# Kernel tuning notes

Measured on AMD Instinct MI355X. Metric: run time of the kernel, lower is better.

## Reference

```python
import jax, jax.numpy as jnp
import numpy as np

N_GRAPHS = 262144
NPG = 6          # players per Rocket League graph
N_NODES = N_GRAPHS * NPG
HIDDEN = 32
FEAT = 4


def _build_edges():
    # fully-connected directed edges within each 6-node graph (30 per graph)
    s, d = np.meshgrid(np.arange(NPG), np.arange(NPG), indexing='ij')
    m = s != d
    ts, td = s[m], d[m]                      # [30]
    off = (np.arange(N_GRAPHS, dtype=np.int64) * NPG)[:, None]
    src = (ts[None, :] + off).reshape(-1)
    dst = (td[None, :] + off).reshape(-1)
    return np.stack([src, dst]).astype(np.int32)  # [2, E]


def setup_inputs() -> dict:
    key = jax.random.key(0)
    ks = jax.random.split(key, 10)
    edge_index = jnp.asarray(_build_edges())
    E = edge_index.shape[1]
    batch = jnp.asarray(np.repeat(np.arange(N_GRAPHS, dtype=np.int32), NPG))
    return {
        'x': jax.random.normal(ks[0], (N_NODES, FEAT), dtype=jnp.float32),
        'edge_index': edge_index,
        'edge_weight': jax.random.uniform(ks[1], (E,), dtype=jnp.float32),
        'batch': batch,
        'W1': jax.random.normal(ks[2], (FEAT, HIDDEN), dtype=jnp.float32) * 0.5,
        'b1': jax.random.normal(ks[3], (HIDDEN,), dtype=jnp.float32) * 0.1,
        'W2': jax.random.normal(ks[4], (HIDDEN, HIDDEN), dtype=jnp.float32) * 0.18,
        'b2': jax.random.normal(ks[5], (HIDDEN,), dtype=jnp.float32) * 0.1,
        'Wo': jax.random.normal(ks[6], (HIDDEN, 1), dtype=jnp.float32) * 0.18,
        'bo': jax.random.normal(ks[7], (1,), dtype=jnp.float32) * 0.1,
        'Wb': jax.random.normal(ks[8], (HIDDEN, 1), dtype=jnp.float32) * 0.18,
        'bb': jax.random.normal(ks[9], (1,), dtype=jnp.float32) * 0.1,
    }


def _gcn_conv(x, W, b, src, dst, w, n_nodes):
    # PyG GCNConv: symmetric normalization with self-loops already appended
    h = x @ W                                            # [N, out]
    deg = jax.ops.segment_sum(w, dst, num_segments=n_nodes)
    dinv = jnp.where(deg > 0, jax.lax.rsqrt(deg), 0.0)
    norm = dinv[src] * w * dinv[dst]                     # [E]
    agg = jax.ops.segment_sum(norm[:, None] * h[src], dst, num_segments=n_nodes)
    return agg + b


def reference(x, edge_index, edge_weight, batch, W1, b1, W2, b2, Wo, bo, Wb, bb):
    n = x.shape[0]
    loop = jnp.arange(n, dtype=edge_index.dtype)
    src = jnp.concatenate([edge_index[0], loop])
    dst = jnp.concatenate([edge_index[1], loop])
    w = jnp.concatenate([edge_weight, jnp.ones((n,), edge_weight.dtype)])

    h = jax.nn.relu(_gcn_conv(x, W1, b1, src, dst, w, n))
    h = jax.nn.relu(_gcn_conv(h, W2, b2, src, dst, w, n))

    # global mean pool by graph
    n_graphs = N_GRAPHS
    sums = jax.ops.segment_sum(h, batch, num_segments=n_graphs)
    cnt = jax.ops.segment_sum(jnp.ones((n,), h.dtype), batch, num_segments=n_graphs)
    pooled = sums / jnp.maximum(cnt, 1.0)[:, None]       # [G, 32]

    orange = jax.nn.sigmoid(pooled @ Wo + bo)            # [G, 1]
    blue = jax.nn.sigmoid(pooled @ Wb + bb)              # [G, 1]
    return orange, blue
```

## Files before the change

kernel.cpp:

```cpp
#include <hip/hip_runtime.h>
#include <hip/hip_bf16.h>

#define G_TOTAL 262144
#define ITERS   2
#define WAVES   4
#define NBLK    4096

typedef short s8v __attribute__((ext_vector_type(8)));
typedef float f4v __attribute__((ext_vector_type(4)));

#define MFMA16(a,b,c) __builtin_amdgcn_mfma_f32_16x16x32_bf16(a,b,c,0,0,0)

__device__ __forceinline__ unsigned short f2bf(float f){
    union { __hip_bfloat16 h; unsigned short u; } cv;
    cv.h = __float2bfloat16(f);
    return cv.u;
}
__device__ __forceinline__ unsigned int pk2(float a, float b){
    return (unsigned int)f2bf(a) | ((unsigned int)f2bf(b) << 16);
}

union FragU { s8v s; uint4 u; };

#define ARENA 7952

__global__ __launch_bounds__(256, 4)
void gcn_wave(const float* __restrict__ x,
              const float* __restrict__ ew,
              const float* __restrict__ W1,
              const float* __restrict__ b1,
              const float* __restrict__ W2,
              const float* __restrict__ b2,
              const float* __restrict__ Wo,
              const float* __restrict__ bo,
              const float* __restrict__ Wb,
              const float* __restrict__ bb,
              float* __restrict__ out)
{
    __shared__ __align__(16) unsigned char LDS[WAVES*ARENA];
    __shared__ float obuf[2][64];

    const int tid = threadIdx.x;
    const int w   = tid >> 6;
    const int l   = tid & 63;
    const int lr  = l & 15;
    const int lq  = l >> 4;

    unsigned char* AR = LDS + w*ARENA;
    unsigned short* h1RW  = (unsigned short*)AR;
    float*          rsumW = (float*)AR;
    unsigned short* actTW = (unsigned short*)(AR + 3456);
    unsigned int*   bandB = (unsigned int*)(AR + 6784);

    #pragma unroll
    for (int i = 0; i < 5; ++i) { const int k = l + 64*i; if (k < 292) bandB[k] = 0u; }

    const int gB = l / 6, dB = l - 6*gB;
    const bool bOK = (l < 48);
    const int gBc = bOK ? gB : 0;
    const int dBc = bOK ? dB : 0;
    int eoff0, eoff1, eoff2, eoff3, eoff4, eoff5;
    {
        int eo[6];
        #pragma unroll
        for (int s = 0; s < 6; ++s)
            eo[s] = (s == dBc) ? gBc*30
                               : gBc*30 + s*5 + (dBc - (dBc > s ? 1 : 0));
        eoff0=eo[0]; eoff1=eo[1]; eoff2=eo[2]; eoff3=eo[3]; eoff4=eo[4]; eoff5=eo[5];
    }
    const int sbB   = 6*gBc;
    const int bcell = bOK ? l : 0;
    int bAddr[3];
    #pragma unroll
    for (int nt = 0; nt < 3; ++nt) {
        const int r  = 16*nt + lr;
        const int g  = r / 6;
        const int s0 = (8*nt + 8*lq - 6*g) >> 1;
        bAddr[nt] = (s0 < -3 || s0 > 2) ? 288 : (6*r + s0);
    }

    s8v w1f[2], w2f[2];
    #pragma unroll
    for (int cn = 0; cn < 2; ++cn) {
        #pragma unroll
        for (int e = 0; e < 8; ++e) {
            const int k = lq*8 + e, col = lr + 16*cn;
            w1f[cn][e] = (k < 4) ? (short)f2bf(W1[k*32 + col]) : (short)0;
            w2f[cn][e] = (short)f2bf(W2[k*32 + col]);
        }
    }
    f4v cb1[2], cb2[2];
    float wor[2][4], wbr[2][4];
    #pragma unroll
    for (int mtc = 0; mtc < 2; ++mtc)
        #pragma unroll
        for (int j = 0; j < 4; ++j) {
            const int ch = 16*mtc + lq*4 + j;
            cb1[mtc][j] = b1[ch];  cb2[mtc][j] = b2[ch];
            wor[mtc][j] = Wo[ch];  wbr[mtc][j] = Wb[ch];
        }
    const float boS = bo[0], bbS = bb[0];

    const long base = (long)blockIdx.x*(32*ITERS) + w*8;

    float evl[2][6];
    uint2 xB[2][3];

    {
        const long gb30 = base*30;
        evl[0][0] = ew[gb30 + eoff0];  evl[0][1] = ew[gb30 + eoff1];
        evl[0][2] = ew[gb30 + eoff2];  evl[0][3] = ew[gb30 + eoff3];
        evl[0][4] = ew[gb30 + eoff4];  evl[0][5] = ew[gb30 + eoff5];
        if (lq == 0) {
            const float* xp = x + base*24;
            #pragma unroll
            for (int mt = 0; mt < 3; ++mt) {
                const float4 xv = *(const float4*)(xp + (16*mt + lr)*4);
                xB[0][mt] = make_uint2(pk2(xv.x, xv.y), pk2(xv.z, xv.w));
            }
        }
    }

    #pragma unroll
    for (int it = 0; it < ITERS; ++it) {
        const int  cbuf = it & 1, nbuf = cbuf ^ 1;
        const long gbW  = base + it*32;

        if (it + 1 < ITERS) {
            const long gb30 = (gbW + 32)*30;
            evl[nbuf][0] = ew[gb30 + eoff0];  evl[nbuf][1] = ew[gb30 + eoff1];
            evl[nbuf][2] = ew[gb30 + eoff2];  evl[nbuf][3] = ew[gb30 + eoff3];
            evl[nbuf][4] = ew[gb30 + eoff4];  evl[nbuf][5] = ew[gb30 + eoff5];
            if (lq == 0) {
                const float* xp = x + (gbW + 32)*24;
                #pragma unroll
                for (int mt = 0; mt < 3; ++mt) {
                    const float4 xv = *(const float4*)(xp + (16*mt + lr)*4);
                    xB[nbuf][mt] = make_uint2(pk2(xv.x, xv.y), pk2(xv.z, xv.w));
                }
            }
        }

        #pragma unroll
        for (int mt = 0; mt < 3; ++mt) {
            s8v a = {0,0,0,0,0,0,0,0};
            if (lq == 0) {
                FragU ua; ua.u = make_uint4(xB[cbuf][mt].x, xB[cbuf][mt].y, 0u, 0u);
                a = ua.s;
            }
            #pragma unroll
            for (int cn = 0; cn < 2; ++cn) {
                f4v z = {0.f,0.f,0.f,0.f};
                f4v t = MFMA16(a, w1f[cn], z);
                *(uint2*)(actTW + (16*cn + lr)*52 + 16*mt + 4*lq) =
                    make_uint2(pk2(t[0],t[1]), pk2(t[2],t[3]));
            }
        }

        {
            const float ws0 = (dB==0) ? 1.0f : evl[cbuf][0];
            const float ws1 = (dB==1) ? 1.0f : evl[cbuf][1];
            const float ws2 = (dB==2) ? 1.0f : evl[cbuf][2];
            const float ws3 = (dB==3) ? 1.0f : evl[cbuf][3];
            const float ws4 = (dB==4) ? 1.0f : evl[cbuf][4];
            const float ws5 = (dB==5) ? 1.0f : evl[cbuf][5];
            const float dd  = rsqrtf(ws0+ws1+ws2+ws3+ws4+ws5);
            const float dv0 = __shfl(dd, sbB+0), dv1 = __shfl(dd, sbB+1);
            const float dv2 = __shfl(dd, sbB+2), dv3 = __shfl(dd, sbB+3);
            const float dv4 = __shfl(dd, sbB+4), dv5 = __shfl(dd, sbB+5);
            if (bOK) {
                *(uint2*)(bandB + bcell*6) =
                    make_uint2(pk2(dd*ws0*dv0, dd*ws1*dv1), pk2(dd*ws2*dv2, dd*ws3*dv3));
                bandB[bcell*6 + 2] = pk2(dd*ws4*dv4, dd*ws5*dv5);
            }
        }

        uint4 bfrv[3];
        #pragma unroll
        for (int nt = 0; nt < 3; ++nt) {
            {
                const unsigned int* bp = bandB + bAddr[nt];
                bfrv[nt] = make_uint4(bp[0], bp[1], bp[2], bp[3]);
            }
            FragU ub; ub.u = bfrv[nt];
            #pragma unroll
            for (int mtc = 0; mtc < 2; ++mtc) {
                FragU ua;
                const unsigned short* ap = actTW + (16*mtc + lr)*52 + 8*nt + 8*lq;
                const uint2 a0 = *(const uint2*)ap;
                const uint2 a1 = *(const uint2*)(ap + 4);
                ua.u = make_uint4(a0.x, a0.y, a1.x, a1.y);
                f4v dD = MFMA16(ua.s, ub.s, cb1[mtc]);
                const float h0 = fmaxf(dD[0], 0.f);
                const float h1v= fmaxf(dD[1], 0.f);
                const float h2v= fmaxf(dD[2], 0.f);
                const float h3v= fmaxf(dD[3], 0.f);
                *(uint2*)(h1RW + (16*nt + lr)*36 + 16*mtc + 4*lq) =
                    make_uint2(pk2(h0,h1v), pk2(h2v,h3v));
            }
        }

        #pragma unroll
        for (int mt = 0; mt < 3; ++mt) {
            FragU ua;
            const unsigned short* hp = h1RW + (16*mt + lr)*36 + 8*lq;
            const uint2 h0 = *(const uint2*)hp;
            const uint2 h1p= *(const uint2*)(hp + 4);
            ua.u = make_uint4(h0.x, h0.y, h1p.x, h1p.y);
            const s8v a = ua.s;
            #pragma unroll
            for (int cn = 0; cn < 2; ++cn) {
                f4v z = {0.f,0.f,0.f,0.f};
                f4v t = MFMA16(a, w2f[cn], z);
                *(uint2*)(actTW + (16*cn + lr)*52 + 16*mt + 4*lq) =
                    make_uint2(pk2(t[0],t[1]), pk2(t[2],t[3]));
            }
        }

        #pragma unroll
        for (int nt = 0; nt < 3; ++nt) {
            FragU ub; ub.u = bfrv[nt];
            float po = 0.f, pb = 0.f;
            #pragma unroll
            for (int mtc = 0; mtc < 2; ++mtc) {
                FragU ua;
                const unsigned short* ap = actTW + (16*mtc + lr)*52 + 8*nt + 8*lq;
                const uint2 a0 = *(const uint2*)ap;
                const uint2 a1 = *(const uint2*)(ap + 4);
                ua.u = make_uint4(a0.x, a0.y, a1.x, a1.y);
                f4v dD = MFMA16(ua.s, ub.s, cb2[mtc]);
                #pragma unroll
                for (int j = 0; j < 4; ++j) {
                    const float h = fmaxf(dD[j], 0.f);
                    po += h * wor[mtc][j];
                    pb += h * wbr[mtc][j];
                }
            }
            po += __shfl_xor(po, 16);  po += __shfl_xor(po, 32);
            pb += __shfl_xor(pb, 16);  pb += __shfl_xor(pb, 32);
            if (lq == 0)      rsumW[16*nt + lr]      = po;
            else if (lq == 1) rsumW[48 + 16*nt + lr] = pb;
        }

        if (l < 16) {
            const int head = l >> 3, gl = l & 7;
            const float* rs = rsumW + head*48 + gl*6;
            const float2 a0 = *(const float2*)rs;
            const float2 a1 = *(const float2*)(rs + 2);
            const float2 a2 = *(const float2*)(rs + 4);
            const float s6 = a0.x+a0.y+a1.x+a1.y+a2.x+a2.y;
            const float zz = s6*(1.f/6.f) + (head ? bbS : boS);
            obuf[head][it*32 + w*8 + gl] = 1.f/(1.f + __expf(-zz));
        }
    }

    __syncthreads();
    if (tid < 128) {
        const int head = tid >> 6, idx = tid & 63;
        out[(long)head*G_TOTAL + (long)blockIdx.x*64 + idx] = obuf[head][idx];
    }
}

extern "C" void kernel_launch(void* const* d_in, const int* in_sizes, int n_in,
                              void* d_out, int out_size, void* d_ws, size_t ws_size,
                              hipStream_t stream)
{
    const float* x  = (const float*)d_in[0];
    const float* ew = (const float*)d_in[2];
    const float* W1 = (const float*)d_in[4];
    const float* b1 = (const float*)d_in[5];
    const float* W2 = (const float*)d_in[6];
    const float* b2 = (const float*)d_in[7];
    const float* Wo = (const float*)d_in[8];
    const float* bo = (const float*)d_in[9];
    const float* Wb = (const float*)d_in[10];
    const float* bb = (const float*)d_in[11];
    float* out = (float*)d_out;

    hipLaunchKernelGGL(gcn_wave, dim3(NBLK), dim3(256), 0, stream,
                       x, ew, W1, b1, W2, b2, Wo, bo, Wb, bb, out);
}
```

Measured before the change: 44.53 us.

## Keep transformed activations in registers and remap band fragments to match

Result: slower. 47.52 us (+6.7%).

```diff
diff --git a/kernel.cpp b/kernel.cpp
--- a/kernel.cpp
+++ b/kernel.cpp
@@ -22,7 +22,7 @@
 
 union FragU { s8v s; uint4 u; };
 
-#define ARENA 7952
+#define ARENA 4624
 
 __global__ __launch_bounds__(256, 4)
 void gcn_wave(const float* __restrict__ x,
@@ -49,8 +49,7 @@
     unsigned char* AR = LDS + w*ARENA;
     unsigned short* h1RW  = (unsigned short*)AR;
     float*          rsumW = (float*)AR;
-    unsigned short* actTW = (unsigned short*)(AR + 3456);
-    unsigned int*   bandB = (unsigned int*)(AR + 6784);
+    unsigned int*   bandB = (unsigned int*)(AR + 3456);
 
     #pragma unroll
     for (int i = 0; i < 5; ++i) { const int k = l + 64*i; if (k < 292) bandB[k] = 0u; }
@@ -70,13 +69,18 @@
     }
     const int sbB   = 6*gBc;
     const int bcell = bOK ? l : 0;
-    int bAddr[3];
+    const bool lq3  = (lq == 3);
+    int bLo[3], bHi[3];
     #pragma unroll
     for (int nt = 0; nt < 3; ++nt) {
+        const int aSel = (nt == 0) ? 0 : ((nt == 2) ? 1 : (lq3 ? 0 : 1));
+        const int bSel = (nt == 0) ? 1 : ((nt == 2) ? 2 : (lq3 ? 1 : 2));
         const int r  = 16*nt + lr;
         const int g  = r / 6;
-        const int s0 = (8*nt + 8*lq - 6*g) >> 1;
-        bAddr[nt] = (s0 < -3 || s0 > 2) ? 288 : (6*r + s0);
+        const int sL = (16*aSel + 4*lq - 6*g) >> 1;
+        const int sH = (16*bSel + 4*lq - 6*g) >> 1;
+        bLo[nt] = (sL < -3 || sL > 4) ? 288 : 6*r + sL;
+        bHi[nt] = (sH < -3 || sH > 4) ? 288 : 6*r + sH;
     }
 
     s8v w1f[2], w2f[2];
@@ -141,6 +145,7 @@
             }
         }
 
+        uint2 t1pk[3][2];
         #pragma unroll
         for (int mt = 0; mt < 3; ++mt) {
             s8v a = {0,0,0,0,0,0,0,0};
@@ -152,8 +157,7 @@
             for (int cn = 0; cn < 2; ++cn) {
                 f4v z = {0.f,0.f,0.f,0.f};
                 f4v t = MFMA16(a, w1f[cn], z);
-                *(uint2*)(actTW + (16*cn + lr)*52 + 16*mt + 4*lq) =
-                    make_uint2(pk2(t[0],t[1]), pk2(t[2],t[3]));
+                t1pk[mt][cn] = make_uint2(pk2(t[0],t[1]), pk2(t[2],t[3]));
             }
         }
 
@@ -178,18 +182,18 @@
         uint4 bfrv[3];
         #pragma unroll
         for (int nt = 0; nt < 3; ++nt) {
-            {
-                const unsigned int* bp = bandB + bAddr[nt];
-                bfrv[nt] = make_uint4(bp[0], bp[1], bp[2], bp[3]);
-            }
+            bfrv[nt] = make_uint4(bandB[bLo[nt]], bandB[bLo[nt]+1],
+                                  bandB[bHi[nt]], bandB[bHi[nt]+1]);
             FragU ub; ub.u = bfrv[nt];
             #pragma unroll
             for (int mtc = 0; mtc < 2; ++mtc) {
-                FragU ua;
-                const unsigned short* ap = actTW + (16*mtc + lr)*52 + 8*nt + 8*lq;
-                const uint2 a0 = *(const uint2*)ap;
-                const uint2 a1 = *(const uint2*)(ap + 4);
-                ua.u = make_uint4(a0.x, a0.y, a1.x, a1.y);
+                const uint2 lo = (nt==0) ? t1pk[0][mtc]
+                               : (nt==2) ? t1pk[1][mtc]
+                               : (lq3 ? t1pk[0][mtc] : t1pk[1][mtc]);
+                const uint2 hi = (nt==0) ? t1pk[1][mtc]
+                               : (nt==2) ? t1pk[2][mtc]
+                               : (lq3 ? t1pk[1][mtc] : t1pk[2][mtc]);
+                FragU ua; ua.u = make_uint4(lo.x, lo.y, hi.x, hi.y);
                 f4v dD = MFMA16(ua.s, ub.s, cb1[mtc]);
                 const float h0 = fmaxf(dD[0], 0.f);
                 const float h1v= fmaxf(dD[1], 0.f);
@@ -200,6 +204,7 @@
             }
         }
 
+        uint2 t2pk[3][2];
         #pragma unroll
         for (int mt = 0; mt < 3; ++mt) {
             FragU ua;
@@ -212,8 +217,7 @@
             for (int cn = 0; cn < 2; ++cn) {
                 f4v z = {0.f,0.f,0.f,0.f};
                 f4v t = MFMA16(a, w2f[cn], z);
-                *(uint2*)(actTW + (16*cn + lr)*52 + 16*mt + 4*lq) =
-                    make_uint2(pk2(t[0],t[1]), pk2(t[2],t[3]));
+                t2pk[mt][cn] = make_uint2(pk2(t[0],t[1]), pk2(t[2],t[3]));
             }
         }
 
@@ -223,11 +227,13 @@
             float po = 0.f, pb = 0.f;
             #pragma unroll
             for (int mtc = 0; mtc < 2; ++mtc) {
-                FragU ua;
-                const unsigned short* ap = actTW + (16*mtc + lr)*52 + 8*nt + 8*lq;
-                const uint2 a0 = *(const uint2*)ap;
-                const uint2 a1 = *(const uint2*)(ap + 4);
-                ua.u = make_uint4(a0.x, a0.y, a1.x, a1.y);
+                const uint2 lo = (nt==0) ? t2pk[0][mtc]
+                               : (nt==2) ? t2pk[1][mtc]
+                               : (lq3 ? t2pk[0][mtc] : t2pk[1][mtc]);
+                const uint2 hi = (nt==0) ? t2pk[1][mtc]
+                               : (nt==2) ? t2pk[2][mtc]
+                               : (lq3 ? t2pk[1][mtc] : t2pk[2][mtc]);
+                FragU ua; ua.u = make_uint4(lo.x, lo.y, hi.x, hi.y);
                 f4v dD = MFMA16(ua.s, ub.s, cb2[mtc]);
                 #pragma unroll
                 for (int j = 0; j < 4; ++j) {
```
